# Performance work log

Measured on AMD Instinct MI355X. Metric: run time of the kernel, lower is better.

The kernel has to match this reference:

```python
import jax, jax.numpy as jnp
import numpy as np

B, N, D = 64, 1024, 128
K = 6  # hardcoded neighbor count in the module


def setup_inputs() -> dict:
    key = jax.random.key(0)
    ks = jax.random.split(key, 11)
    def lin(k, out_d, in_d):
        kw, kb = jax.random.split(k)
        s = 1.0 / np.sqrt(in_d)
        W = jax.random.uniform(kw, (out_d, in_d), minval=-s, maxval=s, dtype=jnp.float32)
        b = jax.random.uniform(kb, (out_d,), minval=-s, maxval=s, dtype=jnp.float32)
        return W, b
    loc = jax.random.uniform(ks[0], (B, N, 2), dtype=jnp.float32)
    deadline = jax.random.uniform(ks[1], (B, N), dtype=jnp.float32)
    depot = jax.random.uniform(ks[2], (B, 2), dtype=jnp.float32)
    W3d, b3d = lin(ks[3], D, 3)
    W2d, b2d = lin(ks[4], D, 2)
    Wnb, bnb = lin(ks[5], D, K * D)
    Wdep, bdep = lin(ks[6], D, 2)
    return {"loc": loc, "deadline": deadline, "depot": depot,
            "W3d": W3d, "b3d": b3d, "W2d": W2d, "b2d": b2d,
            "Wnb": Wnb, "bnb": bnb, "Wdep": Wdep, "bdep": bdep}


def reference(loc, deadline, depot, W3d, b3d, W2d, b2d, Wnb, bnb, Wdep, bdep):
    x = jnp.concatenate([loc, deadline[:, :, None]], axis=2)  # [B,N,3]
    x2 = x[:, :, 0:2]                                          # [B,N,2]
    F2 = jnp.einsum('bnf,df->bnd', x2, W2d) + b2d              # [B,N,D]
    F3 = jnp.einsum('bnf,df->bnd', x, W3d) + b3d               # [B,N,D]
    # pairwise euclidean distances; indices are non-differentiable -> stop_gradient
    diff = x2[:, None, :, :] - x2[:, :, None, :]               # [B,N,N,2]
    dist = jnp.sqrt(jnp.sum(diff * diff, axis=-1))             # [B,N,N]
    _, neighbors = jax.lax.top_k(jax.lax.stop_gradient(-dist), K)  # [B,N,K] smallest dists (incl. self)
    # faithful quirk: original does F0_embedding_2d[:, neighbors][0] == gather from batch-0 embeddings
    nb = F2[0][neighbors]                                      # [B,N,K,D]
    nb_c = nb.reshape(nb.shape[0], nb.shape[1], K * nb.shape[3])  # [B,N,K*D]
    Fn = jnp.einsum('bnf,df->bnd', nb_c, Wnb) + bnb            # [B,N,D]
    Ff = Fn + F3
    dep = depot @ Wdep.T + bdep                                 # [B,D]
    h = jax.nn.leaky_relu(jnp.concatenate([dep[:, None, :], Ff], axis=1), negative_slope=0.01)
    return h, h.mean(axis=1)
```

## Files before the change

### kernel.cpp

```cpp
#include <hip/hip_runtime.h>
#include <hip/hip_bf16.h>

#define CB 64
#define CN 1024
#define CD 128
#define CK 6

typedef __attribute__((ext_vector_type(8))) short short8;
typedef __attribute__((ext_vector_type(4))) float floatx4;

__device__ __forceinline__ unsigned short f2bf(float f) {
    union { float f; unsigned u; } c; c.f = f;
    unsigned u = c.u;
    u += 0x7FFFu + ((u >> 16) & 1u);
    return (unsigned short)(u >> 16);
}

#define WS_G      0
#define WS_NBRS   3145728
#define WS_IDS    3932160
#define WS_STARTS 4063232
#define WS_PART   4129024

struct SortSM { float2 pts[CN]; int cnt[256]; int base[256]; };
struct GSM    { unsigned short As[128 * 40]; unsigned short Bs[128 * 40]; };
union GridSM  { SortSM s; GSM g; };

__global__ void __launch_bounds__(256) k_gridg(
    const float* __restrict__ loc,
    const float* __restrict__ W2d,
    const float* __restrict__ b2d,
    const float* __restrict__ Wnb,
    unsigned short* __restrict__ ids,
    int* __restrict__ starts,
    float* __restrict__ G)
{
    __shared__ GridSM sm;
    int t = threadIdx.x;

    if (blockIdx.x < 64) {
        int b = blockIdx.x;
        const float2* lb = (const float2*)loc + b * CN;
#pragma unroll
        for (int r = 0; r < 4; ++r) sm.s.pts[t + r * 256] = lb[t + r * 256];
        sm.s.cnt[t] = 0;
        __syncthreads();
        int mycell[4];
#pragma unroll
        for (int r = 0; r < 4; ++r) {
            float2 p = sm.s.pts[t * 4 + r];
            int cx = (int)(p.x * 16.0f); cx = cx > 15 ? 15 : cx;
            int cy = (int)(p.y * 16.0f); cy = cy > 15 ? 15 : cy;
            mycell[r] = (cy << 4) + cx;
            atomicAdd(&sm.s.cnt[mycell[r]], 1);
        }
        __syncthreads();
        for (int off = 1; off < 256; off <<= 1) {
            int u = (t >= off) ? sm.s.cnt[t - off] : 0;
            __syncthreads();
            sm.s.cnt[t] += u;
            __syncthreads();
        }
        int excl = (t == 0) ? 0 : sm.s.cnt[t - 1];
        sm.s.base[t] = excl;
        starts[b * 257 + t] = excl;
        if (t == 255) starts[b * 257 + 256] = sm.s.cnt[255];
        __syncthreads();
#pragma unroll
        for (int r = 0; r < 4; ++r) {
            int pos = atomicAdd(&sm.s.base[mycell[r]], 1);
            ids[b * CN + pos] = (unsigned short)(t * 4 + r);
        }
        return;
    }

    int gb = blockIdx.x - 64;
    int k = gb % 6;
    int tile = gb / 6;
    int n0 = tile << 7;

    int wave = t >> 6, lane = t & 63;
    int koff = (lane >> 4) * 8;
    int mrow = lane & 15;

    int e2 = t & 15, rg = t >> 4;
    float2 pl[8];
#pragma unroll
    for (int rr = 0; rr < 8; ++rr)
        pl[rr] = ((const float2*)loc)[n0 + rg + rr * 16];

    int bd = t >> 1, bhalf = t & 1;

    floatx4 acc[2][8];
#pragma unroll
    for (int i = 0; i < 2; ++i)
#pragma unroll
        for (int j = 0; j < 8; ++j) acc[i][j] = (floatx4){0.f, 0.f, 0.f, 0.f};

#pragma unroll
    for (int c = 0; c < 4; ++c) {
        __syncthreads();
        {
            int e0 = c * 32 + e2 * 2;
            float wx0 = W2d[e0 * 2],     wy0 = W2d[e0 * 2 + 1], bz0 = b2d[e0];
            float wx1 = W2d[e0 * 2 + 2], wy1 = W2d[e0 * 2 + 3], bz1 = b2d[e0 + 1];
#pragma unroll
            for (int rr = 0; rr < 8; ++rr) {
                float2 p = pl[rr];
                float v0 = fmaf(p.x, wx0, fmaf(p.y, wy0, bz0));
                float v1 = fmaf(p.x, wx1, fmaf(p.y, wy1, bz1));
                unsigned pack = (unsigned)f2bf(v0) | ((unsigned)f2bf(v1) << 16);
                *(unsigned*)&sm.g.As[(rg + rr * 16) * 40 + e2 * 2] = pack;
            }
        }
        {
            const float* src = Wnb + bd * 768 + k * 128 + c * 32 + bhalf * 16;
            float4 f0 = *(const float4*)(src);
            float4 f1 = *(const float4*)(src + 4);
            float4 f2v = *(const float4*)(src + 8);
            float4 f3 = *(const float4*)(src + 12);
            uint4 o0, o1;
            o0.x = (unsigned)f2bf(f0.x) | ((unsigned)f2bf(f0.y) << 16);
            o0.y = (unsigned)f2bf(f0.z) | ((unsigned)f2bf(f0.w) << 16);
            o0.z = (unsigned)f2bf(f1.x) | ((unsigned)f2bf(f1.y) << 16);
            o0.w = (unsigned)f2bf(f1.z) | ((unsigned)f2bf(f1.w) << 16);
            o1.x = (unsigned)f2bf(f2v.x) | ((unsigned)f2bf(f2v.y) << 16);
            o1.y = (unsigned)f2bf(f2v.z) | ((unsigned)f2bf(f2v.w) << 16);
            o1.z = (unsigned)f2bf(f3.x) | ((unsigned)f2bf(f3.y) << 16);
            o1.w = (unsigned)f2bf(f3.z) | ((unsigned)f2bf(f3.w) << 16);
            *(uint4*)&sm.g.Bs[bd * 40 + bhalf * 16] = o0;
            *(uint4*)&sm.g.Bs[bd * 40 + bhalf * 16 + 8] = o1;
        }
        __syncthreads();
        short8 af[2];
#pragma unroll
        for (int i = 0; i < 2; ++i)
            af[i] = *(const short8*)&sm.g.As[(wave * 32 + i * 16 + mrow) * 40 + koff];
#pragma unroll
        for (int j = 0; j < 8; ++j) {
            short8 bfr = *(const short8*)&sm.g.Bs[(j * 16 + mrow) * 40 + koff];
#pragma unroll
            for (int i = 0; i < 2; ++i)
                acc[i][j] = __builtin_amdgcn_mfma_f32_16x16x32_bf16(
                    af[i], bfr, acc[i][j], 0, 0, 0);
        }
    }

    int lq = lane >> 4, lc = lane & 15;
#pragma unroll
    for (int j = 0; j < 8; ++j) {
        int d = j * 16 + lc;
#pragma unroll
        for (int i = 0; i < 2; ++i) {
#pragma unroll
            for (int r = 0; r < 4; ++r) {
                int row = wave * 32 + i * 16 + lq * 4 + r;
                G[(n0 + row) * 768 + k * 128 + d] = acc[i][j][r];
            }
        }
    }
}

__global__ void __launch_bounds__(256) k_knn(
    const float* __restrict__ loc,
    const unsigned short* __restrict__ ids,
    const int* __restrict__ starts,
    unsigned short* __restrict__ nbrs)
{
    __shared__ float2 xy_tmp[CN];
    __shared__ float2 xy_s[CN];
    __shared__ unsigned short ids_s[CN];
    __shared__ int st_s[257];
    int t = threadIdx.x;
    int b = blockIdx.x >> 4;
    int qbase = (blockIdx.x & 15) << 6;
    const float2* lb = (const float2*)loc + b * CN;
#pragma unroll
    for (int r = 0; r < 4; ++r) {
        int p = t + r * 256;
        xy_tmp[p] = lb[p];
        ids_s[p] = ids[b * CN + p];
    }
    st_s[t] = starts[b * 257 + t];
    if (t == 0) st_s[256] = starts[b * 257 + 256];
    __syncthreads();
#pragma unroll
    for (int r = 0; r < 4; ++r) {
        int p = t + r * 256;
        xy_s[p] = xy_tmp[ids_s[p]];
    }
    __syncthreads();

    int qp = qbase + (t >> 2);
    int pi = t & 3;
    int q = ids_s[qp];
    float2 qxy = xy_s[qp];
    float xq = qxy.x, yq = qxy.y;
    int cx = (int)(xq * 16.0f); cx = cx > 15 ? 15 : cx;
    int cy = (int)(yq * 16.0f); cy = cy > 15 ? 15 : cy;
    float dk[CK]; int ik[CK];
#pragma unroll
    for (int s = 0; s < CK; ++s) { dk[s] = 1e30f; ik[s] = 0x7FFFFFFF; }
    float dk5sq = __builtin_inff();
    const float h = 0.0625f;

#define KNN_CAND(P)                                                        \
    {                                                                      \
        float2 v = xy_s[P];                                                \
        float dx = __fsub_rn(v.x, xq);                                     \
        float dy = __fsub_rn(v.y, yq);                                     \
        float d2 = __fadd_rn(__fmul_rn(dx, dx), __fmul_rn(dy, dy));        \
        if (d2 < dk5sq) {                                                  \
            float ds = __fsqrt_rn(d2);                                     \
            int j = ids_s[P];                                              \
            if (ds < dk[CK - 1] || (ds == dk[CK - 1] && j < ik[CK - 1])) { \
                float dc = ds; int jc = j;                                 \
                _Pragma("unroll")                                          \
                for (int s = 0; s < CK; ++s) {                             \
                    bool sw = (dc < dk[s]) || (dc == dk[s] && jc < ik[s]); \
                    float od = dk[s]; int oi = ik[s];                      \
                    dk[s] = sw ? dc : od; ik[s] = sw ? jc : oi;            \
                    dc = sw ? od : dc;    jc = sw ? oi : jc;               \
                }                                                          \
                if (ik[CK - 1] != 0x7FFFFFFF)                              \
                    dk5sq = __fmul_rn(dk[CK - 1], dk[CK - 1]) * 1.000001f; \
            }                                                              \
        }                                                                  \
    }

    {
        int yl = cy > 0 ? cy - 1 : 0, yh = cy < 15 ? cy + 1 : 15;
        int xl = cx > 0 ? cx - 1 : 0, xh = cx < 15 ? cx + 1 : 15;
        for (int yy = yl; yy <= yh; ++yy) {
            int p  = st_s[(yy << 4) + xl] + pi;
            int pe = st_s[(yy << 4) + xh + 1];
            for (; p < pe; p += 4) KNN_CAND(p)
        }
    }
    bool done;
    {
        int x0 = cx - 1, x1 = cx + 1, y0 = cy - 1, y1 = cy + 1;
        done = (x0 <= 0 && y0 <= 0 && x1 >= 15 && y1 >= 15);
        float mL = x0 > 0  ? __fsub_rn(xq, (float)x0 * h)       : 1e30f;
        float mR = x1 < 15 ? __fsub_rn((float)(x1 + 1) * h, xq) : 1e30f;
        float mB = y0 > 0  ? __fsub_rn(yq, (float)y0 * h)       : 1e30f;
        float mT = y1 < 15 ? __fsub_rn((float)(y1 + 1) * h, yq) : 1e30f;
        float bound = fminf(fminf(mL, mR), fminf(mB, mT)) * 0.999999f;
        done = done || (ik[CK - 1] != 0x7FFFFFFF && dk[CK - 1] < bound);
    }
    if (!done) {
        for (int r = 2; r < 16; ++r) {
            int x0 = cx - r, x1 = cx + r, y0 = cy - r, y1 = cy + r;
            int yl = y0 < 0 ? 0 : y0, yh = y1 > 15 ? 15 : y1;
            int xl = x0 < 0 ? 0 : x0, xh = x1 > 15 ? 15 : x1;
            for (int yy = yl; yy <= yh; ++yy) {
                bool ey = (yy == y0) || (yy == y1);
                if (ey) {
                    int p  = st_s[(yy << 4) + xl] + pi;
                    int pe = st_s[(yy << 4) + xh + 1];
                    for (; p < pe; p += 4) KNN_CAND(p)
                } else {
                    if (x0 >= 0) {
                        int p  = st_s[(yy << 4) + x0] + pi;
                        int pe = st_s[(yy << 4) + x0 + 1];
                        for (; p < pe; p += 4) KNN_CAND(p)
                    }
                    if (x1 <= 15) {
                        int p  = st_s[(yy << 4) + x1] + pi;
                        int pe = st_s[(yy << 4) + x1 + 1];
                        for (; p < pe; p += 4) KNN_CAND(p)
                    }
                }
            }
            if (x0 <= 0 && y0 <= 0 && x1 >= 15 && y1 >= 15) break;
            float mL = x0 > 0  ? __fsub_rn(xq, (float)x0 * h)       : 1e30f;
            float mR = x1 < 15 ? __fsub_rn((float)(x1 + 1) * h, xq) : 1e30f;
            float mB = y0 > 0  ? __fsub_rn(yq, (float)y0 * h)       : 1e30f;
            float mT = y1 < 15 ? __fsub_rn((float)(y1 + 1) * h, yq) : 1e30f;
            float bound = fminf(fminf(mL, mR), fminf(mB, mT)) * 0.999999f;
            if (ik[CK - 1] != 0x7FFFFFFF && dk[CK - 1] < bound) break;
        }
    }
#undef KNN_CAND

#define KNN_MERGE(MASK)                                                     \
    {                                                                       \
        float od[CK]; int oi[CK];                                           \
        _Pragma("unroll")                                                   \
        for (int s = 0; s < CK; ++s) {                                      \
            od[s] = __shfl_xor(dk[s], MASK);                                \
            oi[s] = __shfl_xor(ik[s], MASK);                                \
        }                                                                   \
        _Pragma("unroll")                                                   \
        for (int e = 0; e < CK; ++e) {                                      \
            float dc = od[e]; int jc = oi[e];                               \
            if ((dc < dk[CK - 1]) || (dc == dk[CK - 1] && jc < ik[CK - 1])) { \
                _Pragma("unroll")                                           \
                for (int s = 0; s < CK; ++s) {                              \
                    bool sw = (dc < dk[s]) || (dc == dk[s] && jc < ik[s]);  \
                    float td = dk[s]; int ti = ik[s];                       \
                    dk[s] = sw ? dc : td; ik[s] = sw ? jc : ti;             \
                    dc = sw ? td : dc;    jc = sw ? ti : jc;                \
                }                                                           \
            }                                                               \
        }                                                                   \
    }
    KNN_MERGE(1)
    KNN_MERGE(2)
#undef KNN_MERGE

    if (pi == 0) {
        unsigned short* o = nbrs + (unsigned)(b * CN + q) * CK;
#pragma unroll
        for (int s = 0; s < CK; ++s) o[s] = (unsigned short)ik[s];
    }
}

__global__ void __launch_bounds__(256) k_gather(
    const float* __restrict__ loc,
    const float* __restrict__ dl,
    const unsigned short* __restrict__ nbrs,
    const float* __restrict__ G,
    const float* __restrict__ W3d,
    const float* __restrict__ b3d,
    const float* __restrict__ bnb,
    float* __restrict__ outh,
    float* __restrict__ partials)
{
    __shared__ float psum[4][CD];
    __shared__ unsigned short nbs[64 * CK];
    int t = threadIdx.x, bx = blockIdx.x;
    int rowbase = bx << 6, b = rowbase >> 10;

    if (t < 192)
        ((unsigned*)nbs)[t] = ((const unsigned*)(nbrs + (size_t)rowbase * CK))[t];

    int d4 = t & 31, rg = t >> 5;
    int d0 = d4 * 4;
    float4 w0, w1, w2, bias;
#pragma unroll
    for (int dd = 0; dd < 4; ++dd) {
        int d = d0 + dd;
        ((float*)&w0)[dd] = W3d[d * 3];
        ((float*)&w1)[dd] = W3d[d * 3 + 1];
        ((float*)&w2)[dd] = W3d[d * 3 + 2];
        ((float*)&bias)[dd] = b3d[d] + bnb[d];
    }
    float4 csum = {0.f, 0.f, 0.f, 0.f};
    __syncthreads();

    for (int rr = 0; rr < 8; ++rr) {
        int r = rr * 8 + rg;
        int gr = rowbase + r;
        const unsigned short* nb = nbs + r * CK;
        float4 a = {0.f, 0.f, 0.f, 0.f};
#pragma unroll
        for (int k2 = 0; k2 < CK; ++k2) {
            int m = nb[k2];
            float4 g4 = *(const float4*)(G + m * 768 + k2 * 128 + d0);
            a.x += g4.x; a.y += g4.y; a.z += g4.z; a.w += g4.w;
        }
        float2 l2 = ((const float2*)loc)[gr];
        float dlv = dl[gr];
        float4 v;
        v.x = a.x + bias.x + l2.x * w0.x + l2.y * w1.x + dlv * w2.x;
        v.y = a.y + bias.y + l2.x * w0.y + l2.y * w1.y + dlv * w2.y;
        v.z = a.z + bias.z + l2.x * w0.z + l2.y * w1.z + dlv * w2.z;
        v.w = a.w + bias.w + l2.x * w0.w + l2.y * w1.w + dlv * w2.w;
        float4 lr;
        lr.x = v.x >= 0.f ? v.x : 0.01f * v.x;
        lr.y = v.y >= 0.f ? v.y : 0.01f * v.y;
        lr.z = v.z >= 0.f ? v.z : 0.01f * v.z;
        lr.w = v.w >= 0.f ? v.w : 0.01f * v.w;
        *(float4*)(outh + ((long)b * 1025 + (gr & 1023) + 1) * 128 + d0) = lr;
        csum.x += lr.x; csum.y += lr.y; csum.z += lr.z; csum.w += lr.w;
    }

    csum.x += __shfl_xor(csum.x, 32);
    csum.y += __shfl_xor(csum.y, 32);
    csum.z += __shfl_xor(csum.z, 32);
    csum.w += __shfl_xor(csum.w, 32);
    int wave = t >> 6, lane = t & 63;
    if (lane < 32) *(float4*)&psum[wave][d0] = csum;
    __syncthreads();
    if (t < CD)
        partials[(bx << 7) + t] =
            psum[0][t] + psum[1][t] + psum[2][t] + psum[3][t];
}

__global__ void k_fin(const float* __restrict__ depot,
                      const float* __restrict__ Wdep,
                      const float* __restrict__ bdep,
                      const float* __restrict__ partials,
                      float* __restrict__ out) {
    int idx = blockIdx.x * 256 + threadIdx.x;
    int b = idx >> 7, d = idx & 127;
    float acc = 0.f;
#pragma unroll
    for (int g = 0; g < 16; ++g) acc += partials[(b * 16 + g) * 128 + d];
    float dv = depot[b * 2] * Wdep[d * 2] + depot[b * 2 + 1] * Wdep[d * 2 + 1] + bdep[d];
    float lr = dv >= 0.f ? dv : 0.01f * dv;
    out[(long)b * 1025 * 128 + d] = lr;
    out[(long)CB * 1025 * 128 + idx] = (acc + lr) * (1.0f / 1025.0f);
}

extern "C" void kernel_launch(void* const* d_in, const int* in_sizes, int n_in,
                              void* d_out, int out_size, void* d_ws, size_t ws_size,
                              hipStream_t stream) {
    const float* loc      = (const float*)d_in[0];
    const float* deadline = (const float*)d_in[1];
    const float* depot    = (const float*)d_in[2];
    const float* W3d      = (const float*)d_in[3];
    const float* b3d      = (const float*)d_in[4];
    const float* W2d      = (const float*)d_in[5];
    const float* b2d      = (const float*)d_in[6];
    const float* Wnb      = (const float*)d_in[7];
    const float* bnb      = (const float*)d_in[8];
    const float* Wdep     = (const float*)d_in[9];
    const float* bdep     = (const float*)d_in[10];
    float* out = (float*)d_out;

    char* ws = (char*)d_ws;
    float* G              = (float*)(ws + WS_G);
    unsigned short* nbrs  = (unsigned short*)(ws + WS_NBRS);
    unsigned short* ids   = (unsigned short*)(ws + WS_IDS);
    int* starts           = (int*)(ws + WS_STARTS);
    float* partials       = (float*)(ws + WS_PART);

    k_gridg<<<112, 256, 0, stream>>>(loc, W2d, b2d, Wnb, ids, starts, G);
    k_knn<<<1024, 256, 0, stream>>>(loc, ids, starts, nbrs);
    k_gather<<<1024, 256, 0, stream>>>(loc, deadline, nbrs, G, W3d, b3d, bnb,
                                       out, partials);
    k_fin<<<32, 256, 0, stream>>>(depot, Wdep, bdep, partials, out);
}
```

Measured before the change: 136.5 us.

## Merge kNN lane partials before ring search and fuse final reduction into gather

The kNN search now merges the four lanes' partial top-6 lists after the 3x3 cell scan, so the tighter shared bound can end the ring expansion early. The expansion runs only when some query in the wave still needs it, and a duplicate-aware merge follows. The separate k_fin kernel is removed: gather blocks atomically add per-batch sums, and the last block per batch writes the depot row and the mean. This saves one kernel launch and reduces kNN work, at the cost of atomics and extra shuffle-merge steps.

```diff
diff --git a/kernel.cpp b/kernel.cpp
--- a/kernel.cpp
+++ b/kernel.cpp
@@ -20,7 +20,8 @@
 #define WS_NBRS   3145728
 #define WS_IDS    3932160
 #define WS_STARTS 4063232
-#define WS_PART   4129024
+#define WS_BSUM   4129024
+#define WS_CNT    4161792
 
 struct SortSM { float2 pts[CN]; int cnt[256]; int base[256]; };
 struct GSM    { unsigned short As[128 * 40]; unsigned short Bs[128 * 40]; };
@@ -33,13 +34,17 @@
     const float* __restrict__ Wnb,
     unsigned short* __restrict__ ids,
     int* __restrict__ starts,
-    float* __restrict__ G)
+    float* __restrict__ G,
+    float* __restrict__ bsum,
+    int* __restrict__ cnt)
 {
     __shared__ GridSM sm;
     int t = threadIdx.x;
 
     if (blockIdx.x < 64) {
         int b = blockIdx.x;
+        if (t < 128) bsum[(b << 7) + t] = 0.f;
+        if (t == 128) cnt[b] = 0;
         const float2* lb = (const float2*)loc + b * CN;
 #pragma unroll
         for (int r = 0; r < 4; ++r) sm.s.pts[t + r * 256] = lb[t + r * 256];
@@ -228,61 +233,6 @@
         }                                                                  \
     }
 
-    {
-        int yl = cy > 0 ? cy - 1 : 0, yh = cy < 15 ? cy + 1 : 15;
-        int xl = cx > 0 ? cx - 1 : 0, xh = cx < 15 ? cx + 1 : 15;
-        for (int yy = yl; yy <= yh; ++yy) {
-            int p  = st_s[(yy << 4) + xl] + pi;
-            int pe = st_s[(yy << 4) + xh + 1];
-            for (; p < pe; p += 4) KNN_CAND(p)
-        }
-    }
-    bool done;
-    {
-        int x0 = cx - 1, x1 = cx + 1, y0 = cy - 1, y1 = cy + 1;
-        done = (x0 <= 0 && y0 <= 0 && x1 >= 15 && y1 >= 15);
-        float mL = x0 > 0  ? __fsub_rn(xq, (float)x0 * h)       : 1e30f;
-        float mR = x1 < 15 ? __fsub_rn((float)(x1 + 1) * h, xq) : 1e30f;
-        float mB = y0 > 0  ? __fsub_rn(yq, (float)y0 * h)       : 1e30f;
-        float mT = y1 < 15 ? __fsub_rn((float)(y1 + 1) * h, yq) : 1e30f;
-        float bound = fminf(fminf(mL, mR), fminf(mB, mT)) * 0.999999f;
-        done = done || (ik[CK - 1] != 0x7FFFFFFF && dk[CK - 1] < bound);
-    }
-    if (!done) {
-        for (int r = 2; r < 16; ++r) {
-            int x0 = cx - r, x1 = cx + r, y0 = cy - r, y1 = cy + r;
-            int yl = y0 < 0 ? 0 : y0, yh = y1 > 15 ? 15 : y1;
-            int xl = x0 < 0 ? 0 : x0, xh = x1 > 15 ? 15 : x1;
-            for (int yy = yl; yy <= yh; ++yy) {
-                bool ey = (yy == y0) || (yy == y1);
-                if (ey) {
-                    int p  = st_s[(yy << 4) + xl] + pi;
-                    int pe = st_s[(yy << 4) + xh + 1];
-                    for (; p < pe; p += 4) KNN_CAND(p)
-                } else {
-                    if (x0 >= 0) {
-                        int p  = st_s[(yy << 4) + x0] + pi;
-                        int pe = st_s[(yy << 4) + x0 + 1];
-                        for (; p < pe; p += 4) KNN_CAND(p)
-                    }
-                    if (x1 <= 15) {
-                        int p  = st_s[(yy << 4) + x1] + pi;
-                        int pe = st_s[(yy << 4) + x1 + 1];
-                        for (; p < pe; p += 4) KNN_CAND(p)
-                    }
-                }
-            }
-            if (x0 <= 0 && y0 <= 0 && x1 >= 15 && y1 >= 15) break;
-            float mL = x0 > 0  ? __fsub_rn(xq, (float)x0 * h)       : 1e30f;
-            float mR = x1 < 15 ? __fsub_rn((float)(x1 + 1) * h, xq) : 1e30f;
-            float mB = y0 > 0  ? __fsub_rn(yq, (float)y0 * h)       : 1e30f;
-            float mT = y1 < 15 ? __fsub_rn((float)(y1 + 1) * h, yq) : 1e30f;
-            float bound = fminf(fminf(mL, mR), fminf(mB, mT)) * 0.999999f;
-            if (ik[CK - 1] != 0x7FFFFFFF && dk[CK - 1] < bound) break;
-        }
-    }
-#undef KNN_CAND
-
 #define KNN_MERGE(MASK)                                                     \
     {                                                                       \
         float od[CK]; int oi[CK];                                           \
@@ -305,9 +255,101 @@
             }                                                               \
         }                                                                   \
     }
+
+#define KNN_MERGE_D(MASK)                                                   \
+    {                                                                       \
+        float od[CK]; int oi[CK];                                           \
+        _Pragma("unroll")                                                   \
+        for (int s = 0; s < CK; ++s) {                                      \
+            od[s] = __shfl_xor(dk[s], MASK);                                \
+            oi[s] = __shfl_xor(ik[s], MASK);                                \
+        }                                                                   \
+        _Pragma("unroll")                                                   \
+        for (int e = 0; e < CK; ++e) {                                      \
+            float dc = od[e]; int jc = oi[e];                               \
+            bool dup = false;                                               \
+            _Pragma("unroll")                                               \
+            for (int s = 0; s < CK; ++s) dup = dup || (jc == ik[s]);        \
+            if (!dup &&                                                     \
+                ((dc < dk[CK - 1]) || (dc == dk[CK - 1] && jc < ik[CK - 1]))) { \
+                _Pragma("unroll")                                           \
+                for (int s = 0; s < CK; ++s) {                              \
+                    bool sw = (dc < dk[s]) || (dc == dk[s] && jc < ik[s]);  \
+                    float td = dk[s]; int ti = ik[s];                       \
+                    dk[s] = sw ? dc : td; ik[s] = sw ? jc : ti;             \
+                    dc = sw ? td : dc;    jc = sw ? ti : jc;                \
+                }                                                           \
+            }                                                               \
+        }                                                                   \
+    }
+
+    {
+        int yl = cy > 0 ? cy - 1 : 0, yh = cy < 15 ? cy + 1 : 15;
+        int xl = cx > 0 ? cx - 1 : 0, xh = cx < 15 ? cx + 1 : 15;
+        for (int yy = yl; yy <= yh; ++yy) {
+            int p  = st_s[(yy << 4) + xl] + pi;
+            int pe = st_s[(yy << 4) + xh + 1];
+            for (; p < pe; p += 4) KNN_CAND(p)
+        }
+    }
+
     KNN_MERGE(1)
     KNN_MERGE(2)
+
+    bool done;
+    {
+        int x0 = cx - 1, x1 = cx + 1, y0 = cy - 1, y1 = cy + 1;
+        done = (x0 <= 0 && y0 <= 0 && x1 >= 15 && y1 >= 15);
+        float mL = x0 > 0  ? __fsub_rn(xq, (float)x0 * h)       : 1e30f;
+        float mR = x1 < 15 ? __fsub_rn((float)(x1 + 1) * h, xq) : 1e30f;
+        float mB = y0 > 0  ? __fsub_rn(yq, (float)y0 * h)       : 1e30f;
+        float mT = y1 < 15 ? __fsub_rn((float)(y1 + 1) * h, yq) : 1e30f;
+        float bound = fminf(fminf(mL, mR), fminf(mB, mT)) * 0.999999f;
+        done = done || (ik[CK - 1] != 0x7FFFFFFF && dk[CK - 1] < bound);
+    }
+
+    if (__any(!done)) {
+        if (!done) {
+            if (ik[CK - 1] != 0x7FFFFFFF)
+                dk5sq = __fmul_rn(dk[CK - 1], dk[CK - 1]) * 1.000001f;
+            for (int r = 2; r < 16; ++r) {
+                int x0 = cx - r, x1 = cx + r, y0 = cy - r, y1 = cy + r;
+                int yl = y0 < 0 ? 0 : y0, yh = y1 > 15 ? 15 : y1;
+                int xl = x0 < 0 ? 0 : x0, xh = x1 > 15 ? 15 : x1;
+                for (int yy = yl; yy <= yh; ++yy) {
+                    bool ey = (yy == y0) || (yy == y1);
+                    if (ey) {
+                        int p  = st_s[(yy << 4) + xl] + pi;
+                        int pe = st_s[(yy << 4) + xh + 1];
+                        for (; p < pe; p += 4) KNN_CAND(p)
+                    } else {
+                        if (x0 >= 0) {
+                            int p  = st_s[(yy << 4) + x0] + pi;
+                            int pe = st_s[(yy << 4) + x0 + 1];
+                            for (; p < pe; p += 4) KNN_CAND(p)
+                        }
+                        if (x1 <= 15) {
+                            int p  = st_s[(yy << 4) + x1] + pi;
+                            int pe = st_s[(yy << 4) + x1 + 1];
+                            for (; p < pe; p += 4) KNN_CAND(p)
+                        }
+                    }
+                }
+                if (x0 <= 0 && y0 <= 0 && x1 >= 15 && y1 >= 15) break;
+                float mL = x0 > 0  ? __fsub_rn(xq, (float)x0 * h)       : 1e30f;
+                float mR = x1 < 15 ? __fsub_rn((float)(x1 + 1) * h, xq) : 1e30f;
+                float mB = y0 > 0  ? __fsub_rn(yq, (float)y0 * h)       : 1e30f;
+                float mT = y1 < 15 ? __fsub_rn((float)(y1 + 1) * h, yq) : 1e30f;
+                float bound = fminf(fminf(mL, mR), fminf(mB, mT)) * 0.999999f;
+                if (ik[CK - 1] != 0x7FFFFFFF && dk[CK - 1] < bound) break;
+            }
+        }
+        KNN_MERGE_D(1)
+        KNN_MERGE_D(2)
+    }
+#undef KNN_CAND
 #undef KNN_MERGE
+#undef KNN_MERGE_D
 
     if (pi == 0) {
         unsigned short* o = nbrs + (unsigned)(b * CN + q) * CK;
@@ -316,7 +358,7 @@
     }
 }
 
-__global__ void __launch_bounds__(256) k_gather(
+__global__ void __launch_bounds__(256) k_gatherfin(
     const float* __restrict__ loc,
     const float* __restrict__ dl,
     const unsigned short* __restrict__ nbrs,
@@ -324,11 +366,16 @@
     const float* __restrict__ W3d,
     const float* __restrict__ b3d,
     const float* __restrict__ bnb,
-    float* __restrict__ outh,
-    float* __restrict__ partials)
+    const float* __restrict__ depot,
+    const float* __restrict__ Wdep,
+    const float* __restrict__ bdep,
+    float* __restrict__ out,
+    float* __restrict__ bsum,
+    int* __restrict__ cnt)
 {
     __shared__ float psum[4][CD];
     __shared__ unsigned short nbs[64 * CK];
+    __shared__ int lastflag;
     int t = threadIdx.x, bx = blockIdx.x;
     int rowbase = bx << 6, b = rowbase >> 10;
 
@@ -372,7 +419,7 @@
         lr.y = v.y >= 0.f ? v.y : 0.01f * v.y;
         lr.z = v.z >= 0.f ? v.z : 0.01f * v.z;
         lr.w = v.w >= 0.f ? v.w : 0.01f * v.w;
-        *(float4*)(outh + ((long)b * 1025 + (gr & 1023) + 1) * 128 + d0) = lr;
+        *(float4*)(out + ((long)b * 1025 + (gr & 1023) + 1) * 128 + d0) = lr;
         csum.x += lr.x; csum.y += lr.y; csum.z += lr.z; csum.w += lr.w;
     }
 
@@ -384,24 +431,24 @@
     if (lane < 32) *(float4*)&psum[wave][d0] = csum;
     __syncthreads();
     if (t < CD)
-        partials[(bx << 7) + t] =
-            psum[0][t] + psum[1][t] + psum[2][t] + psum[3][t];
-}
-
-__global__ void k_fin(const float* __restrict__ depot,
-                      const float* __restrict__ Wdep,
-                      const float* __restrict__ bdep,
-                      const float* __restrict__ partials,
-                      float* __restrict__ out) {
-    int idx = blockIdx.x * 256 + threadIdx.x;
-    int b = idx >> 7, d = idx & 127;
-    float acc = 0.f;
-#pragma unroll
-    for (int g = 0; g < 16; ++g) acc += partials[(b * 16 + g) * 128 + d];
-    float dv = depot[b * 2] * Wdep[d * 2] + depot[b * 2 + 1] * Wdep[d * 2 + 1] + bdep[d];
-    float lr = dv >= 0.f ? dv : 0.01f * dv;
-    out[(long)b * 1025 * 128 + d] = lr;
-    out[(long)CB * 1025 * 128 + idx] = (acc + lr) * (1.0f / 1025.0f);
+        atomicAdd(bsum + (b << 7) + t,
+                  psum[0][t] + psum[1][t] + psum[2][t] + psum[3][t]);
+    __syncthreads();
+    if (t == 0) {
+        __threadfence();
+        int old = atomicAdd(cnt + b, 1);
+        lastflag = (old == 15);
+    }
+    __syncthreads();
+    if (lastflag && t < CD) {
+        float acc = atomicAdd(bsum + (b << 7) + t, 0.0f);
+        float dv = depot[b * 2] * Wdep[t * 2] + depot[b * 2 + 1] * Wdep[t * 2 + 1]
+                 + bdep[t];
+        float lr = dv >= 0.f ? dv : 0.01f * dv;
+        out[(long)b * 1025 * 128 + t] = lr;
+        out[(long)CB * 1025 * 128 + (b << 7) + t] =
+            (acc + lr) * (1.0f / 1025.0f);
+    }
 }
 
 extern "C" void kernel_launch(void* const* d_in, const int* in_sizes, int n_in,
@@ -425,11 +472,13 @@
     unsigned short* nbrs  = (unsigned short*)(ws + WS_NBRS);
     unsigned short* ids   = (unsigned short*)(ws + WS_IDS);
     int* starts           = (int*)(ws + WS_STARTS);
-    float* partials       = (float*)(ws + WS_PART);
-
-    k_gridg<<<112, 256, 0, stream>>>(loc, W2d, b2d, Wnb, ids, starts, G);
+    float* bsum           = (float*)(ws + WS_BSUM);
+    int* cnt              = (int*)(ws + WS_CNT);
+
+    k_gridg<<<112, 256, 0, stream>>>(loc, W2d, b2d, Wnb, ids, starts, G,
+                                     bsum, cnt);
     k_knn<<<1024, 256, 0, stream>>>(loc, ids, starts, nbrs);
-    k_gather<<<1024, 256, 0, stream>>>(loc, deadline, nbrs, G, W3d, b3d, bnb,
-                                       out, partials);
-    k_fin<<<32, 256, 0, stream>>>(depot, Wdep, bdep, partials, out);
+    k_gatherfin<<<1024, 256, 0, stream>>>(loc, deadline, nbrs, G, W3d, b3d,
+                                          bnb, depot, Wdep, bdep, out,
+                                          bsum, cnt);
 }
```

After: 152.7 us. 11.9% more time.

## Store gather table in bf16 and process rows in spatially sorted order

Applied to the files above, without the earlier changes.

The precomputed per-neighbor projection table G is now written as bf16 instead of fp32, which halves the bytes each gathered row costs. The gather kernel visits query rows in grid-cell order via the ids permutation, so neighbouring queries share G rows and get better cache locality. Each thread now handles 8 columns and two rows per iteration with all twelve loads issued up front for more memory-level parallelism. Rounding G to bf16 adds error to the neighbor term, and output writes become scattered rows instead of contiguous ones.

```diff
diff --git a/kernel.cpp b/kernel.cpp
--- a/kernel.cpp
+++ b/kernel.cpp
@@ -14,6 +14,15 @@
     unsigned u = c.u;
     u += 0x7FFFu + ((u >> 16) & 1u);
     return (unsigned short)(u >> 16);
+}
+__device__ __forceinline__ float bf2f(unsigned short u) {
+    union { unsigned u; float f; } c; c.u = ((unsigned)u) << 16; return c.f;
+}
+__device__ __forceinline__ float bfe(const uint4& g, int dd) {
+    unsigned w = (&g.x)[dd >> 1];
+    unsigned short h = (dd & 1) ? (unsigned short)(w >> 16)
+                                : (unsigned short)(w & 0xFFFFu);
+    return bf2f(h);
 }
 
 #define WS_G      0
@@ -33,7 +42,7 @@
     const float* __restrict__ Wnb,
     unsigned short* __restrict__ ids,
     int* __restrict__ starts,
-    float* __restrict__ G)
+    unsigned short* __restrict__ G16)
 {
     __shared__ GridSM sm;
     int t = threadIdx.x;
@@ -155,7 +164,7 @@
 #pragma unroll
             for (int r = 0; r < 4; ++r) {
                 int row = wave * 32 + i * 16 + lq * 4 + r;
-                G[(n0 + row) * 768 + k * 128 + d] = acc[i][j][r];
+                G16[(n0 + row) * 768 + k * 128 + d] = f2bf(acc[i][j][r]);
             }
         }
     }
@@ -320,7 +329,8 @@
     const float* __restrict__ loc,
     const float* __restrict__ dl,
     const unsigned short* __restrict__ nbrs,
-    const float* __restrict__ G,
+    const unsigned short* __restrict__ ids,
+    const unsigned short* __restrict__ G16,
     const float* __restrict__ W3d,
     const float* __restrict__ b3d,
     const float* __restrict__ bnb,
@@ -329,59 +339,109 @@
 {
     __shared__ float psum[4][CD];
     __shared__ unsigned short nbs[64 * CK];
+    __shared__ unsigned short nloc[64];
     int t = threadIdx.x, bx = blockIdx.x;
-    int rowbase = bx << 6, b = rowbase >> 10;
-
-    if (t < 192)
-        ((unsigned*)nbs)[t] = ((const unsigned*)(nbrs + (size_t)rowbase * CK))[t];
-
-    int d4 = t & 31, rg = t >> 5;
-    int d0 = d4 * 4;
-    float4 w0, w1, w2, bias;
-#pragma unroll
-    for (int dd = 0; dd < 4; ++dd) {
+    int b = bx >> 4;
+    int qbase = (bx & 15) << 6;
+
+    if (t < 32)
+        ((unsigned*)nloc)[t] = ((const unsigned*)(ids + b * CN + qbase))[t];
+    __syncthreads();
+    if (t < 64) {
+        int n = nloc[t];
+        const unsigned short* src = nbrs + ((size_t)(b << 10) + n) * CK;
+#pragma unroll
+        for (int s = 0; s < CK; ++s) nbs[t * CK + s] = src[s];
+    }
+
+    int d8 = t & 15, rg = t >> 4;
+    int d0 = d8 * 8;
+    float w0[8], w1[8], w2[8], bias[8];
+#pragma unroll
+    for (int dd = 0; dd < 8; ++dd) {
         int d = d0 + dd;
-        ((float*)&w0)[dd] = W3d[d * 3];
-        ((float*)&w1)[dd] = W3d[d * 3 + 1];
-        ((float*)&w2)[dd] = W3d[d * 3 + 2];
-        ((float*)&bias)[dd] = b3d[d] + bnb[d];
-    }
-    float4 csum = {0.f, 0.f, 0.f, 0.f};
+        w0[dd] = W3d[d * 3];
+        w1[dd] = W3d[d * 3 + 1];
+        w2[dd] = W3d[d * 3 + 2];
+        bias[dd] = b3d[d] + bnb[d];
+    }
+    float csum[8];
+#pragma unroll
+    for (int dd = 0; dd < 8; ++dd) csum[dd] = 0.f;
     __syncthreads();
 
-    for (int rr = 0; rr < 8; ++rr) {
-        int r = rr * 8 + rg;
-        int gr = rowbase + r;
-        const unsigned short* nb = nbs + r * CK;
-        float4 a = {0.f, 0.f, 0.f, 0.f};
-#pragma unroll
-        for (int k2 = 0; k2 < CK; ++k2) {
-            int m = nb[k2];
-            float4 g4 = *(const float4*)(G + m * 768 + k2 * 128 + d0);
-            a.x += g4.x; a.y += g4.y; a.z += g4.z; a.w += g4.w;
-        }
-        float2 l2 = ((const float2*)loc)[gr];
-        float dlv = dl[gr];
-        float4 v;
-        v.x = a.x + bias.x + l2.x * w0.x + l2.y * w1.x + dlv * w2.x;
-        v.y = a.y + bias.y + l2.x * w0.y + l2.y * w1.y + dlv * w2.y;
-        v.z = a.z + bias.z + l2.x * w0.z + l2.y * w1.z + dlv * w2.z;
-        v.w = a.w + bias.w + l2.x * w0.w + l2.y * w1.w + dlv * w2.w;
-        float4 lr;
-        lr.x = v.x >= 0.f ? v.x : 0.01f * v.x;
-        lr.y = v.y >= 0.f ? v.y : 0.01f * v.y;
-        lr.z = v.z >= 0.f ? v.z : 0.01f * v.z;
-        lr.w = v.w >= 0.f ? v.w : 0.01f * v.w;
-        *(float4*)(outh + ((long)b * 1025 + (gr & 1023) + 1) * 128 + d0) = lr;
-        csum.x += lr.x; csum.y += lr.y; csum.z += lr.z; csum.w += lr.w;
-    }
-
-    csum.x += __shfl_xor(csum.x, 32);
-    csum.y += __shfl_xor(csum.y, 32);
-    csum.z += __shfl_xor(csum.z, 32);
-    csum.w += __shfl_xor(csum.w, 32);
+#pragma unroll
+    for (int rr = 0; rr < 2; ++rr) {
+        int r0 = rr * 32 + rg;
+        int r1 = r0 + 16;
+        int n0s = nloc[r0], n1s = nloc[r1];
+        int gr0 = (b << 10) + n0s, gr1 = (b << 10) + n1s;
+        const unsigned short* nA = nbs + r0 * CK;
+        const unsigned short* nB = nbs + r1 * CK;
+        uint4 ga0 = *(const uint4*)(G16 + nA[0] * 768 + 0 * 128 + d0);
+        uint4 ga1 = *(const uint4*)(G16 + nA[1] * 768 + 1 * 128 + d0);
+        uint4 ga2 = *(const uint4*)(G16 + nA[2] * 768 + 2 * 128 + d0);
+        uint4 ga3 = *(const uint4*)(G16 + nA[3] * 768 + 3 * 128 + d0);
+        uint4 ga4 = *(const uint4*)(G16 + nA[4] * 768 + 4 * 128 + d0);
+        uint4 ga5 = *(const uint4*)(G16 + nA[5] * 768 + 5 * 128 + d0);
+        uint4 gb0 = *(const uint4*)(G16 + nB[0] * 768 + 0 * 128 + d0);
+        uint4 gb1 = *(const uint4*)(G16 + nB[1] * 768 + 1 * 128 + d0);
+        uint4 gb2 = *(const uint4*)(G16 + nB[2] * 768 + 2 * 128 + d0);
+        uint4 gb3 = *(const uint4*)(G16 + nB[3] * 768 + 3 * 128 + d0);
+        uint4 gb4 = *(const uint4*)(G16 + nB[4] * 768 + 4 * 128 + d0);
+        uint4 gb5 = *(const uint4*)(G16 + nB[5] * 768 + 5 * 128 + d0);
+        float2 lA = ((const float2*)loc)[gr0];
+        float2 lB = ((const float2*)loc)[gr1];
+        float dA = dl[gr0];
+        float dB = dl[gr1];
+        {
+            float o[8];
+#pragma unroll
+            for (int dd = 0; dd < 8; ++dd) {
+                float a = ((((bfe(ga0, dd) + bfe(ga1, dd)) + bfe(ga2, dd))
+                           + bfe(ga3, dd)) + bfe(ga4, dd)) + bfe(ga5, dd);
+                float v = a + bias[dd] + lA.x * w0[dd] + lA.y * w1[dd]
+                        + dA * w2[dd];
+                o[dd] = v >= 0.f ? v : 0.01f * v;
+                csum[dd] += o[dd];
+            }
+            float* ob = outh + ((long)b * 1025 + n0s + 1) * 128 + d0;
+            float4 s0, s1;
+            s0.x = o[0]; s0.y = o[1]; s0.z = o[2]; s0.w = o[3];
+            s1.x = o[4]; s1.y = o[5]; s1.z = o[6]; s1.w = o[7];
+            *(float4*)(ob) = s0;
+            *(float4*)(ob + 4) = s1;
+        }
+        {
+            float o[8];
+#pragma unroll
+            for (int dd = 0; dd < 8; ++dd) {
+                float a = ((((bfe(gb0, dd) + bfe(gb1, dd)) + bfe(gb2, dd))
+                           + bfe(gb3, dd)) + bfe(gb4, dd)) + bfe(gb5, dd);
+                float v = a + bias[dd] + lB.x * w0[dd] + lB.y * w1[dd]
+                        + dB * w2[dd];
+                o[dd] = v >= 0.f ? v : 0.01f * v;
+                csum[dd] += o[dd];
+            }
+            float* ob = outh + ((long)b * 1025 + n1s + 1) * 128 + d0;
+            float4 s0, s1;
+            s0.x = o[0]; s0.y = o[1]; s0.z = o[2]; s0.w = o[3];
+            s1.x = o[4]; s1.y = o[5]; s1.z = o[6]; s1.w = o[7];
+            *(float4*)(ob) = s0;
+            *(float4*)(ob + 4) = s1;
+        }
+    }
+
+#pragma unroll
+    for (int dd = 0; dd < 8; ++dd) {
+        csum[dd] += __shfl_xor(csum[dd], 16);
+        csum[dd] += __shfl_xor(csum[dd], 32);
+    }
     int wave = t >> 6, lane = t & 63;
-    if (lane < 32) *(float4*)&psum[wave][d0] = csum;
+    if (lane < 16) {
+#pragma unroll
+        for (int dd = 0; dd < 8; ++dd) psum[wave][d0 + dd] = csum[dd];
+    }
     __syncthreads();
     if (t < CD)
         partials[(bx << 7) + t] =
@@ -421,15 +481,15 @@
     float* out = (float*)d_out;
 
     char* ws = (char*)d_ws;
-    float* G              = (float*)(ws + WS_G);
+    unsigned short* G16   = (unsigned short*)(ws + WS_G);
     unsigned short* nbrs  = (unsigned short*)(ws + WS_NBRS);
     unsigned short* ids   = (unsigned short*)(ws + WS_IDS);
     int* starts           = (int*)(ws + WS_STARTS);
     float* partials       = (float*)(ws + WS_PART);
 
-    k_gridg<<<112, 256, 0, stream>>>(loc, W2d, b2d, Wnb, ids, starts, G);
+    k_gridg<<<112, 256, 0, stream>>>(loc, W2d, b2d, Wnb, ids, starts, G16);
     k_knn<<<1024, 256, 0, stream>>>(loc, ids, starts, nbrs);
-    k_gather<<<1024, 256, 0, stream>>>(loc, deadline, nbrs, G, W3d, b3d, bnb,
-                                       out, partials);
+    k_gather<<<1024, 256, 0, stream>>>(loc, deadline, nbrs, ids, G16, W3d,
+                                       b3d, bnb, out, partials);
     k_fin<<<32, 256, 0, stream>>>(depot, Wdep, bdep, partials, out);
 }
```

New measurement: 134.0 us. About the same (-1.8%).
